# Optimization experiments

Measured on AMD Instinct MI355X. Metric: run time of the kernel, lower is better.

The kernel has to match this reference:

```python
import jax, jax.numpy as jnp
import numpy as np


def setup_inputs() -> dict:
    key = jax.random.key(0)
    k1, k2 = jax.random.split(key)
    N, C, H, W = 8, 64, 256, 256
    out_h, out_w = 256, 256
    U = jax.random.normal(k1, (N, C, H, W), dtype=jnp.float32)
    theta = jax.random.normal(k2, (N, 2, out_h * out_w), dtype=jnp.float32)
    return {"U": U, "theta": theta, "out_h": out_h, "out_w": out_w}


def reference(U, theta, out_h, out_w):
    N, C, H, W = U.shape
    HWo = out_h * out_w
    # identity normalized grid in [-1,1], x varies along width, y along height
    x_lin = jnp.linspace(-1.0, 1.0, out_w, dtype=U.dtype)
    y_lin = jnp.linspace(-1.0, 1.0, out_h, dtype=U.dtype)
    x_t = jnp.broadcast_to(x_lin[None, :], (out_h, out_w)).reshape(-1)
    y_t = jnp.broadcast_to(y_lin[:, None], (out_h, out_w)).reshape(-1)
    grid = jnp.stack([x_t, y_t], axis=0)            # [2, HWo]
    T_g = theta + grid[None, :, :]                  # [N, 2, HWo]
    x = T_g[:, 0, :].reshape(-1)                    # [N*HWo]
    y = T_g[:, 1, :].reshape(-1)
    # map to pixel coordinates
    x = (x + 1.0) * (W - 1) / 2.0
    y = (y + 1.0) * (H - 1) / 2.0
    x0 = jnp.clip(jnp.floor(x).astype(jnp.int32), 0, W - 2)
    x1 = jnp.clip(jnp.ceil(x).astype(jnp.int32), 0, W - 1)
    y0 = jnp.clip(jnp.floor(y).astype(jnp.int32), 0, H - 2)
    y1 = jnp.clip(jnp.ceil(y).astype(jnp.int32), 0, H - 1)
    base = jnp.repeat(jnp.arange(N, dtype=jnp.int32) * (H * W), HWo)
    idx_a = base + y0 * W + x0
    idx_b = base + y1 * W + x0
    idx_c = base + y0 * W + x1
    idx_d = base + y1 * W + x1
    # faithful to original: flat view of NCHW memory as rows of length C
    im_flat = U.reshape(-1, C)                      # [N*H*W, C]
    Ia = im_flat[idx_a]
    Ib = im_flat[idx_b]
    Ic = im_flat[idx_c]
    Id = im_flat[idx_d]
    x0f, x1f = x0.astype(U.dtype), x1.astype(U.dtype)
    y0f, y1f = y0.astype(U.dtype), y1.astype(U.dtype)
    wa = ((x1f - x) * (y1f - y))[:, None]
    wb = ((x1f - x) * (y - y0f))[:, None]
    wc = ((x - x0f) * (y1f - y))[:, None]
    wd = ((x - x0f) * (y - y0f))[:, None]
    out = wa * Ia + wb * Ib + wc * Ic + wd * Id     # [N*HWo, C]
    return out.reshape(N, C, out_h, out_w)
```

## Files before the change

### kernel.cpp

```cpp
#include <hip/hip_runtime.h>

constexpr int N   = 8;
constexpr int C   = 64;
constexpr int H   = 256;
constexpr int W   = 256;
constexpr int OH  = 256;
constexpr int OW  = 256;
constexpr int HWo = OH * OW;

typedef float f32x4 __attribute__((ext_vector_type(4)));

__global__ __launch_bounds__(256) void stn_kernel(
    const float* __restrict__ U,
    const float* __restrict__ theta,
    float* __restrict__ out)
{
    const int t  = blockIdx.x * blockDim.x + threadIdx.x;
    const int s  = t >> 4;
    const int cg = (t & 15) << 2;

    const int n  = s >> 16;
    const int p  = s & (HWo - 1);
    const int ow = p & (OW - 1);
    const int oh = p >> 8;

    const float gx = (float)ow * (2.0f / 255.0f) - 1.0f;
    const float gy = (float)oh * (2.0f / 255.0f) - 1.0f;

    float x = theta[(n * 2 + 0) * HWo + p] + gx;
    float y = theta[(n * 2 + 1) * HWo + p] + gy;

    x = (x + 1.0f) * (float)(W - 1) * 0.5f;
    y = (y + 1.0f) * (float)(H - 1) * 0.5f;

    const int x0 = min(max((int)floorf(x), 0), W - 2);
    const int x1 = min(max((int)ceilf(x),  0), W - 1);
    const int y0 = min(max((int)floorf(y), 0), H - 2);
    const int y1 = min(max((int)ceilf(y),  0), H - 1);

    const float x0f = (float)x0, x1f = (float)x1;
    const float y0f = (float)y0, y1f = (float)y1;

    const float wa = (x1f - x) * (y1f - y);
    const float wb = (x1f - x) * (y - y0f);
    const float wc = (x - x0f) * (y1f - y);
    const float wd = (x - x0f) * (y - y0f);

    const int base = n * (H * W);
    const int ia = (base + y0 * W + x0) * C + cg;
    const int ib = (base + y1 * W + x0) * C + cg;
    const int ic = (base + y0 * W + x1) * C + cg;
    const int id = (base + y1 * W + x1) * C + cg;

    const f32x4 A  = *(const f32x4*)(U + ia);
    const f32x4 B  = *(const f32x4*)(U + ib);
    const f32x4 Cv = *(const f32x4*)(U + ic);
    const f32x4 D  = *(const f32x4*)(U + id);

    f32x4 o = wa * A + wb * B + wc * Cv + wd * D;

    __builtin_nontemporal_store(o, (f32x4*)(out + (size_t)s * C + cg));
}

extern "C" void kernel_launch(void* const* d_in, const int* in_sizes, int n_in,
                              void* d_out, int out_size, void* d_ws, size_t ws_size,
                              hipStream_t stream)
{
    const float* U     = (const float*)d_in[0];
    const float* theta = (const float*)d_in[1];
    float* out         = (float*)d_out;

    const int total   = N * HWo * 16;
    const int block   = 256;
    const int grid    = total / block;

    stn_kernel<<<grid, block, 0, stream>>>(U, theta, out);
}
```

Baseline: 54.42 us.

## Process two samples per thread and remap blocks contiguously per XCD

Each thread now handles two adjacent output samples. It loads theta as float2 and issues eight 16-byte gathers before the blends, aiming for more memory-level parallelism and fewer threads. Block IDs are remapped so each XCD works on a contiguous range of samples, which should improve L2 locality of the gathered input rows. In exchange, register pressure rises and the grid is halved, which may lower occupancy.

```diff
diff --git a/kernel.cpp b/kernel.cpp
--- a/kernel.cpp
+++ b/kernel.cpp
@@ -7,6 +7,10 @@
 constexpr int OH  = 256;
 constexpr int OW  = 256;
 constexpr int HWo = OH * OW;
+constexpr int SAMPLES = N * HWo;
+constexpr int BLOCK   = 256;
+constexpr int GRID    = SAMPLES / 2 * 16 / BLOCK;
+constexpr int GRID_PER_XCD = GRID / 8;
 
 typedef float f32x4 __attribute__((ext_vector_type(4)));
 
@@ -15,51 +19,74 @@
     const float* __restrict__ theta,
     float* __restrict__ out)
 {
-    const int t  = blockIdx.x * blockDim.x + threadIdx.x;
-    const int s  = t >> 4;
+    const int b  = blockIdx.x;
+    const int bs = (b & 7) * GRID_PER_XCD + (b >> 3);
+
+    const int t  = bs * BLOCK + threadIdx.x;
+    const int q  = t >> 4;
     const int cg = (t & 15) << 2;
 
-    const int n  = s >> 16;
-    const int p  = s & (HWo - 1);
-    const int ow = p & (OW - 1);
-    const int oh = p >> 8;
+    const int s0 = q << 1;
+    const int n  = s0 >> 16;
+    const int p0 = s0 & (HWo - 1);
+    const int ow0 = p0 & (OW - 1);
+    const int oh0 = p0 >> 8;
 
-    const float gx = (float)ow * (2.0f / 255.0f) - 1.0f;
-    const float gy = (float)oh * (2.0f / 255.0f) - 1.0f;
+    const float2 tx = *(const float2*)(theta + (size_t)(n * 2 + 0) * HWo + p0);
+    const float2 ty = *(const float2*)(theta + (size_t)(n * 2 + 1) * HWo + p0);
 
-    float x = theta[(n * 2 + 0) * HWo + p] + gx;
-    float y = theta[(n * 2 + 1) * HWo + p] + gy;
+    const float gx0 = (float)ow0 * (2.0f / 255.0f) - 1.0f;
+    const float gx1 = (float)(ow0 + 1) * (2.0f / 255.0f) - 1.0f;
+    const float gy  = (float)oh0 * (2.0f / 255.0f) - 1.0f;
 
-    x = (x + 1.0f) * (float)(W - 1) * 0.5f;
-    y = (y + 1.0f) * (float)(H - 1) * 0.5f;
+    float xA = (tx.x + gx0 + 1.0f) * (float)(W - 1) * 0.5f;
+    float xB = (tx.y + gx1 + 1.0f) * (float)(W - 1) * 0.5f;
+    float yA = (ty.x + gy  + 1.0f) * (float)(H - 1) * 0.5f;
+    float yB = (ty.y + gy  + 1.0f) * (float)(H - 1) * 0.5f;
 
-    const int x0 = min(max((int)floorf(x), 0), W - 2);
-    const int x1 = min(max((int)ceilf(x),  0), W - 1);
-    const int y0 = min(max((int)floorf(y), 0), H - 2);
-    const int y1 = min(max((int)ceilf(y),  0), H - 1);
-
-    const float x0f = (float)x0, x1f = (float)x1;
-    const float y0f = (float)y0, y1f = (float)y1;
-
-    const float wa = (x1f - x) * (y1f - y);
-    const float wb = (x1f - x) * (y - y0f);
-    const float wc = (x - x0f) * (y1f - y);
-    const float wd = (x - x0f) * (y - y0f);
+    const int x0A = min(max((int)floorf(xA), 0), W - 2);
+    const int x1A = min(max((int)ceilf(xA),  0), W - 1);
+    const int y0A = min(max((int)floorf(yA), 0), H - 2);
+    const int y1A = min(max((int)ceilf(yA),  0), H - 1);
+    const int x0B = min(max((int)floorf(xB), 0), W - 2);
+    const int x1B = min(max((int)ceilf(xB),  0), W - 1);
+    const int y0B = min(max((int)floorf(yB), 0), H - 2);
+    const int y1B = min(max((int)ceilf(yB),  0), H - 1);
 
     const int base = n * (H * W);
-    const int ia = (base + y0 * W + x0) * C + cg;
-    const int ib = (base + y1 * W + x0) * C + cg;
-    const int ic = (base + y0 * W + x1) * C + cg;
-    const int id = (base + y1 * W + x1) * C + cg;
+    const int iaA = (base + y0A * W + x0A) * C + cg;
+    const int ibA = (base + y1A * W + x0A) * C + cg;
+    const int icA = (base + y0A * W + x1A) * C + cg;
+    const int idA = (base + y1A * W + x1A) * C + cg;
+    const int iaB = (base + y0B * W + x0B) * C + cg;
+    const int ibB = (base + y1B * W + x0B) * C + cg;
+    const int icB = (base + y0B * W + x1B) * C + cg;
+    const int idB = (base + y1B * W + x1B) * C + cg;
 
-    const f32x4 A  = *(const f32x4*)(U + ia);
-    const f32x4 B  = *(const f32x4*)(U + ib);
-    const f32x4 Cv = *(const f32x4*)(U + ic);
-    const f32x4 D  = *(const f32x4*)(U + id);
+    const f32x4 Aa = *(const f32x4*)(U + iaA);
+    const f32x4 Ba = *(const f32x4*)(U + ibA);
+    const f32x4 Ca = *(const f32x4*)(U + icA);
+    const f32x4 Da = *(const f32x4*)(U + idA);
+    const f32x4 Ab = *(const f32x4*)(U + iaB);
+    const f32x4 Bb = *(const f32x4*)(U + ibB);
+    const f32x4 Cb = *(const f32x4*)(U + icB);
+    const f32x4 Db = *(const f32x4*)(U + idB);
 
-    f32x4 o = wa * A + wb * B + wc * Cv + wd * D;
+    const float waA = ((float)x1A - xA) * ((float)y1A - yA);
+    const float wbA = ((float)x1A - xA) * (yA - (float)y0A);
+    const float wcA = (xA - (float)x0A) * ((float)y1A - yA);
+    const float wdA = (xA - (float)x0A) * (yA - (float)y0A);
+    const float waB = ((float)x1B - xB) * ((float)y1B - yB);
+    const float wbB = ((float)x1B - xB) * (yB - (float)y0B);
+    const float wcB = (xB - (float)x0B) * ((float)y1B - yB);
+    const float wdB = (xB - (float)x0B) * (yB - (float)y0B);
 
-    __builtin_nontemporal_store(o, (f32x4*)(out + (size_t)s * C + cg));
+    const f32x4 oA = waA * Aa + wbA * Ba + wcA * Ca + wdA * Da;
+    const f32x4 oB = waB * Ab + wbB * Bb + wcB * Cb + wdB * Db;
+
+    float* outp = out + (size_t)s0 * C + cg;
+    __builtin_nontemporal_store(oA, (f32x4*)outp);
+    __builtin_nontemporal_store(oB, (f32x4*)(outp + C));
 }
 
 extern "C" void kernel_launch(void* const* d_in, const int* in_sizes, int n_in,
@@ -70,9 +97,5 @@
     const float* theta = (const float*)d_in[1];
     float* out         = (float*)d_out;
 
-    const int total   = N * HWo * 16;
-    const int block   = 256;
-    const int grid    = total / block;
-
-    stn_kernel<<<grid, block, 0, stream>>>(U, theta, out);
+    stn_kernel<<<GRID, BLOCK, 0, stream>>>(U, theta, out);
 }
```

Measured after the change: 46.90 us. -13.8%, faster.

## Process four samples per thread and remap blocks across XCDs

Applied to the files above, without the earlier changes.

Each thread now handles four consecutive output samples for one channel group. It loads theta as float4 vectors and issues all sixteen gather loads before any blending, which raises memory-level parallelism. Block indices are also remapped so that consecutive blocks, which touch nearby image regions, land on the same XCD and can share L2. The cost is more registers per thread and a quarter as many threads, which can lower occupancy.

```diff
diff --git a/kernel.cpp b/kernel.cpp
--- a/kernel.cpp
+++ b/kernel.cpp
@@ -7,6 +7,10 @@
 constexpr int OH  = 256;
 constexpr int OW  = 256;
 constexpr int HWo = OH * OW;
+constexpr int SPT = 4;
+constexpr int BLOCK = 256;
+constexpr int GRID  = (N * HWo / SPT) * 16 / BLOCK;
+constexpr int GRID_PER_XCD = GRID / 8;
 
 typedef float f32x4 __attribute__((ext_vector_type(4)));
 
@@ -15,51 +19,62 @@
     const float* __restrict__ theta,
     float* __restrict__ out)
 {
-    const int t  = blockIdx.x * blockDim.x + threadIdx.x;
-    const int s  = t >> 4;
+    const int b  = blockIdx.x;
+    const int bs = (b & 7) * GRID_PER_XCD + (b >> 3);
+
+    const int t  = bs * BLOCK + threadIdx.x;
+    const int q  = t >> 4;
     const int cg = (t & 15) << 2;
 
-    const int n  = s >> 16;
-    const int p  = s & (HWo - 1);
-    const int ow = p & (OW - 1);
-    const int oh = p >> 8;
+    const int s0  = q << 2;
+    const int n   = s0 >> 16;
+    const int p0  = s0 & (HWo - 1);
+    const int ow0 = p0 & (OW - 1);
+    const int oh0 = p0 >> 8;
 
-    const float gx = (float)ow * (2.0f / 255.0f) - 1.0f;
-    const float gy = (float)oh * (2.0f / 255.0f) - 1.0f;
+    const f32x4 tx = *(const f32x4*)(theta + (size_t)(n * 2 + 0) * HWo + p0);
+    const f32x4 ty = *(const f32x4*)(theta + (size_t)(n * 2 + 1) * HWo + p0);
 
-    float x = theta[(n * 2 + 0) * HWo + p] + gx;
-    float y = theta[(n * 2 + 1) * HWo + p] + gy;
+    const float gy   = (float)oh0 * (2.0f / 255.0f) - 1.0f;
+    const int   base = n * (H * W);
 
-    x = (x + 1.0f) * (float)(W - 1) * 0.5f;
-    y = (y + 1.0f) * (float)(H - 1) * 0.5f;
+    int   idx[SPT][4];
+    float wgt[SPT][4];
+#pragma unroll
+    for (int k = 0; k < SPT; ++k) {
+        const float gx = (float)(ow0 + k) * (2.0f / 255.0f) - 1.0f;
+        const float x = (tx[k] + gx + 1.0f) * 127.5f;
+        const float y = (ty[k] + gy + 1.0f) * 127.5f;
+        const int x0 = min(max((int)floorf(x), 0), W - 2);
+        const int x1 = min(max((int)ceilf(x),  0), W - 1);
+        const int y0 = min(max((int)floorf(y), 0), H - 2);
+        const int y1 = min(max((int)ceilf(y),  0), H - 1);
+        idx[k][0] = (base + y0 * W + x0) * C + cg;
+        idx[k][1] = (base + y1 * W + x0) * C + cg;
+        idx[k][2] = (base + y0 * W + x1) * C + cg;
+        idx[k][3] = (base + y1 * W + x1) * C + cg;
+        const float dx1 = (float)x1 - x, dx0 = x - (float)x0;
+        const float dy1 = (float)y1 - y, dy0 = y - (float)y0;
+        wgt[k][0] = dx1 * dy1;
+        wgt[k][1] = dx1 * dy0;
+        wgt[k][2] = dx0 * dy1;
+        wgt[k][3] = dx0 * dy0;
+    }
 
-    const int x0 = min(max((int)floorf(x), 0), W - 2);
-    const int x1 = min(max((int)ceilf(x),  0), W - 1);
-    const int y0 = min(max((int)floorf(y), 0), H - 2);
-    const int y1 = min(max((int)ceilf(y),  0), H - 1);
+    f32x4 v[SPT][4];
+#pragma unroll
+    for (int k = 0; k < SPT; ++k)
+#pragma unroll
+        for (int j = 0; j < 4; ++j)
+            v[k][j] = *(const f32x4*)(U + idx[k][j]);
 
-    const float x0f = (float)x0, x1f = (float)x1;
-    const float y0f = (float)y0, y1f = (float)y1;
-
-    const float wa = (x1f - x) * (y1f - y);
-    const float wb = (x1f - x) * (y - y0f);
-    const float wc = (x - x0f) * (y1f - y);
-    const float wd = (x - x0f) * (y - y0f);
-
-    const int base = n * (H * W);
-    const int ia = (base + y0 * W + x0) * C + cg;
-    const int ib = (base + y1 * W + x0) * C + cg;
-    const int ic = (base + y0 * W + x1) * C + cg;
-    const int id = (base + y1 * W + x1) * C + cg;
-
-    const f32x4 A  = *(const f32x4*)(U + ia);
-    const f32x4 B  = *(const f32x4*)(U + ib);
-    const f32x4 Cv = *(const f32x4*)(U + ic);
-    const f32x4 D  = *(const f32x4*)(U + id);
-
-    f32x4 o = wa * A + wb * B + wc * Cv + wd * D;
-
-    __builtin_nontemporal_store(o, (f32x4*)(out + (size_t)s * C + cg));
+    float* outp = out + (size_t)s0 * C + cg;
+#pragma unroll
+    for (int k = 0; k < SPT; ++k) {
+        const f32x4 o = wgt[k][0] * v[k][0] + wgt[k][1] * v[k][1]
+                      + wgt[k][2] * v[k][2] + wgt[k][3] * v[k][3];
+        __builtin_nontemporal_store(o, (f32x4*)(outp + k * C));
+    }
 }
 
 extern "C" void kernel_launch(void* const* d_in, const int* in_sizes, int n_in,
@@ -70,9 +85,5 @@
     const float* theta = (const float*)d_in[1];
     float* out         = (float*)d_out;
 
-    const int total   = N * HWo * 16;
-    const int block   = 256;
-    const int grid    = total / block;
-
-    stn_kernel<<<grid, block, 0, stream>>>(U, theta, out);
+    stn_kernel<<<GRID, BLOCK, 0, stream>>>(U, theta, out);
 }
```

Measured after the change: 47.00 us. 1.16x faster.
